# Kernel tuning notes

Measured on AMD Instinct MI355X. Metric: run time of the kernel, lower is better.

## Reference

```python
import jax, jax.numpy as jnp
import numpy as np


def setup_inputs() -> dict:
    key = jax.random.key(0)
    kx, ky = jax.random.split(key)
    B, N, C, G = 16, 8192, 64, 512
    x = jax.random.normal(kx, (B, N, C), dtype=jnp.float32)
    y = jax.random.randint(ky, (B, N), 0, G).astype(jnp.int64)
    return {"x": x, "y": y, "g": G}


def reference(x, y, g):
    # x: [B, N, C], y: [B, N] group ids (y < 0 -> dropped via sentinel class g)
    N = x.shape[1]
    y = jnp.where(y < 0, g, y)
    # one_hot over g+1 classes, drop the sentinel column -> [B, N, G]
    oh = jax.nn.one_hot(y, g + 1, dtype=x.dtype)[..., :g]
    # (x[:, :, None, :] * oh[..., None]).mean(1)  ==  einsum / N
    feature = jnp.einsum('bng,bnc->bgc', oh, x) / N  # [B, G, C]
    mask = oh.sum(axis=1) > 0                        # [B, G]
    return feature, mask
```

## Files before the change

kernel.cpp:

```cpp
#include <hip/hip_runtime.h>


#define B_ 16
#define N_ 8192
#define C_ 64
#define G_ 512

__global__ __launch_bounds__(256) void gap_gather(const float* __restrict__ x,
                                                  const int* __restrict__ y,
                                                  float* __restrict__ feature,
                                                  float* __restrict__ maskout) {
    const int lane = threadIdx.x & 63;
    const int wid  = (blockIdx.x * blockDim.x + threadIdx.x) >> 6;
    const int b = wid >> 9;
    const int g = wid & (G_ - 1);

    const int*   yb = y + b * N_;
    const float* xb = x + (size_t)b * (size_t)(N_ * C_);

    float acc = 0.0f;
    int   cnt = 0;

    for (int n0 = 0; n0 < N_; n0 += 256) {
        const int4 yv = *reinterpret_cast<const int4*>(yb + n0 + lane * 4);
        unsigned long long m0 = __ballot(yv.x == g);
        unsigned long long m1 = __ballot(yv.y == g);
        unsigned long long m2 = __ballot(yv.z == g);
        unsigned long long m3 = __ballot(yv.w == g);
        cnt += __popcll(m0) + __popcll(m1) + __popcll(m2) + __popcll(m3);
        while (m0) { int l = __builtin_ctzll(m0); m0 &= m0 - 1;
                     acc += xb[(size_t)(n0 + l * 4 + 0) * C_ + lane]; }
        while (m1) { int l = __builtin_ctzll(m1); m1 &= m1 - 1;
                     acc += xb[(size_t)(n0 + l * 4 + 1) * C_ + lane]; }
        while (m2) { int l = __builtin_ctzll(m2); m2 &= m2 - 1;
                     acc += xb[(size_t)(n0 + l * 4 + 2) * C_ + lane]; }
        while (m3) { int l = __builtin_ctzll(m3); m3 &= m3 - 1;
                     acc += xb[(size_t)(n0 + l * 4 + 3) * C_ + lane]; }
    }

    feature[((size_t)b * G_ + g) * C_ + lane] = acc * (1.0f / (float)N_);
    if (lane == 0) maskout[b * G_ + g] = (cnt > 0) ? 1.0f : 0.0f;
}

extern "C" void kernel_launch(void* const* d_in, const int* in_sizes, int n_in,
                              void* d_out, int out_size, void* d_ws, size_t ws_size,
                              hipStream_t stream) {
    const float* x = (const float*)d_in[0];
    const int*   y = (const int*)d_in[1];
    float* feature = (float*)d_out;
    float* maskout = (float*)d_out + (size_t)B_ * G_ * C_;

    const int total_waves = B_ * G_;
    const int block = 256;
    const int grid  = total_waves * 64 / block;
    gap_gather<<<grid, block, 0, stream>>>(x, y, feature, maskout);
}
```

Baseline: 89.87 us.

## Replace per-group gather scan with segmented LDS atomic scatter plus reduction pass

The old kernel gave each (batch, group) pair its own wave, and every wave rescanned all of y for its batch, so the label array was read G times per batch. The new version splits each batch into 16 segments. Each 1024-thread block streams its slice of x once with float4 loads and scatter-adds rows into a padded 512x68 LDS accumulator using shared-memory atomics, while also counting group sizes. A second kernel sums the 16 partial results from workspace and writes the mean and the mask. The cost is about 139 KB of LDS per block, an extra workspace round-trip and a second launch, plus float atomic contention on LDS.

```diff
diff --git a/kernel.cpp b/kernel.cpp
--- a/kernel.cpp
+++ b/kernel.cpp
@@ -5,41 +5,83 @@
 #define N_ 8192
 #define C_ 64
 #define G_ 512
+#define S_ 16
+#define SEG (N_ / S_)
+#define STRIDE 68
+#define LDS_FLOATS (G_ * STRIDE + G_)
+#define LDS_BYTES (LDS_FLOATS * 4)
 
-__global__ __launch_bounds__(256) void gap_gather(const float* __restrict__ x,
-                                                  const int* __restrict__ y,
-                                                  float* __restrict__ feature,
-                                                  float* __restrict__ maskout) {
-    const int lane = threadIdx.x & 63;
-    const int wid  = (blockIdx.x * blockDim.x + threadIdx.x) >> 6;
-    const int b = wid >> 9;
-    const int g = wid & (G_ - 1);
+__global__ __launch_bounds__(1024)
+void gap_phase1(const float* __restrict__ x, const int* __restrict__ y,
+                float* __restrict__ pfeat, float* __restrict__ pcnt) {
+    const int t = threadIdx.x;
+    const int b = blockIdx.x >> 4;
+    const int s = blockIdx.x & (S_ - 1);
 
-    const int*   yb = y + b * N_;
-    const float* xb = x + (size_t)b * (size_t)(N_ * C_);
+    extern __shared__ float lds[];
+    float* lacc = lds;
+    int*   lcnt = (int*)(lds + G_ * STRIDE);
 
-    float acc = 0.0f;
-    int   cnt = 0;
+    for (int i = t; i < LDS_FLOATS; i += 1024) ((int*)lds)[i] = 0;
+    __syncthreads();
 
-    for (int n0 = 0; n0 < N_; n0 += 256) {
-        const int4 yv = *reinterpret_cast<const int4*>(yb + n0 + lane * 4);
-        unsigned long long m0 = __ballot(yv.x == g);
-        unsigned long long m1 = __ballot(yv.y == g);
-        unsigned long long m2 = __ballot(yv.z == g);
-        unsigned long long m3 = __ballot(yv.w == g);
-        cnt += __popcll(m0) + __popcll(m1) + __popcll(m2) + __popcll(m3);
-        while (m0) { int l = __builtin_ctzll(m0); m0 &= m0 - 1;
-                     acc += xb[(size_t)(n0 + l * 4 + 0) * C_ + lane]; }
-        while (m1) { int l = __builtin_ctzll(m1); m1 &= m1 - 1;
-                     acc += xb[(size_t)(n0 + l * 4 + 1) * C_ + lane]; }
-        while (m2) { int l = __builtin_ctzll(m2); m2 &= m2 - 1;
-                     acc += xb[(size_t)(n0 + l * 4 + 2) * C_ + lane]; }
-        while (m3) { int l = __builtin_ctzll(m3); m3 &= m3 - 1;
-                     acc += xb[(size_t)(n0 + l * 4 + 3) * C_ + lane]; }
+    const float4* xseg = (const float4*)(x + ((size_t)b * N_ + (size_t)s * SEG) * C_);
+    const int*    yseg = y + b * N_ + s * SEG;
+
+    float4 v[8]; int g[8];
+    #pragma unroll
+    for (int i = 0; i < 8; ++i) v[i] = xseg[i * 1024 + t];
+    #pragma unroll
+    for (int i = 0; i < 8; ++i) g[i] = yseg[(i * 1024 + t) >> 4];
+
+    #pragma unroll
+    for (int i = 0; i < 8; ++i) {
+        const int gi = g[i];
+        if (gi >= 0 && gi < G_) {
+            float* p = &lacc[gi * STRIDE + ((i * 1024 + t) & 15) * 4];
+            atomicAdd(p + 0, v[i].x);
+            atomicAdd(p + 1, v[i].y);
+            atomicAdd(p + 2, v[i].z);
+            atomicAdd(p + 3, v[i].w);
+        }
     }
+    if (t < SEG) {
+        const int gg = yseg[t];
+        if (gg >= 0 && gg < G_) atomicAdd(&lcnt[gg], 1);
+    }
+    __syncthreads();
 
-    feature[((size_t)b * G_ + g) * C_ + lane] = acc * (1.0f / (float)N_);
-    if (lane == 0) maskout[b * G_ + g] = (cnt > 0) ? 1.0f : 0.0f;
+    float4* pf = (float4*)(pfeat + (size_t)(b * S_ + s) * G_ * C_);
+    #pragma unroll
+    for (int i = 0; i < 8; ++i) {
+        const int idx4 = i * 1024 + t;
+        pf[idx4] = *(const float4*)&lacc[(idx4 >> 4) * STRIDE + (idx4 & 15) * 4];
+    }
+    if (t < G_) pcnt[(b * S_ + s) * G_ + t] = (float)lcnt[t];
+}
+
+__global__ __launch_bounds__(1024)
+void gap_phase2(const float* __restrict__ pfeat, const float* __restrict__ pcnt,
+                float* __restrict__ feature, float* __restrict__ maskout) {
+    const int gid = blockIdx.x * 1024 + threadIdx.x;
+    if (gid < B_ * G_ * C_) {
+        const int b   = gid >> 15;
+        const int rem = gid & (G_ * C_ - 1);
+        const float* p = pfeat + (size_t)b * S_ * G_ * C_ + rem;
+        float sum = 0.f;
+        #pragma unroll
+        for (int s = 0; s < S_; ++s) sum += p[(size_t)s * G_ * C_];
+        feature[gid] = sum * (1.0f / (float)N_);
+    } else if (gid < B_ * G_ * C_ + B_ * G_) {
+        const int m = gid - B_ * G_ * C_;
+        const int b = m >> 9;
+        const int g = m & (G_ - 1);
+        const float* p = pcnt + (size_t)b * S_ * G_ + g;
+        float c = 0.f;
+        #pragma unroll
+        for (int s = 0; s < S_; ++s) c += p[s * G_];
+        maskout[m] = (c > 0.f) ? 1.0f : 0.0f;
+    }
 }
 
 extern "C" void kernel_launch(void* const* d_in, const int* in_sizes, int n_in,
@@ -48,10 +90,15 @@
     const float* x = (const float*)d_in[0];
     const int*   y = (const int*)d_in[1];
     float* feature = (float*)d_out;
-    float* maskout = (float*)d_out + (size_t)B_ * G_ * C_;
+    float* maskout = feature + (size_t)B_ * G_ * C_;
+    float* pfeat   = (float*)d_ws;
+    float* pcnt    = pfeat + (size_t)B_ * S_ * G_ * C_;
 
-    const int total_waves = B_ * G_;
-    const int block = 256;
-    const int grid  = total_waves * 64 / block;
-    gap_gather<<<grid, block, 0, stream>>>(x, y, feature, maskout);
+    (void)hipFuncSetAttribute(reinterpret_cast<const void*>(gap_phase1),
+                              hipFuncAttributeMaxDynamicSharedMemorySize, LDS_BYTES);
+
+    gap_phase1<<<B_ * S_, 1024, LDS_BYTES, stream>>>(x, y, pfeat, pcnt);
+
+    const int total = B_ * G_ * C_ + B_ * G_;
+    gap_phase2<<<(total + 1023) / 1024, 1024, 0, stream>>>(pfeat, pcnt, feature, maskout);
 }
```

New measurement: 126.8 us. +41.1%, slower.
